# Performance work log

Measured on AMD Instinct MI355X. Metric: run time of the kernel, lower is better.

Reference implementation:

```python
import jax, jax.numpy as jnp
import numpy as np

N_COMPONENTS = 16
N_FEATURES = 64
N_SAMPLES = 200000


def setup_inputs() -> dict:
    key = jax.random.key(0)
    k_data, k_means, k_cov = jax.random.split(key, 3)
    data = jax.random.normal(k_data, (N_SAMPLES, N_FEATURES), dtype=jnp.float32)
    weights = jnp.ones((N_COMPONENTS,), dtype=jnp.float32) / N_COMPONENTS
    means = jax.random.normal(k_means, (N_COMPONENTS, N_FEATURES), dtype=jnp.float32)
    # SPD covariances: A A^T / d + I (module inits to identity; use realistic SPD here)
    A = jax.random.normal(k_cov, (N_COMPONENTS, N_FEATURES, N_FEATURES), dtype=jnp.float32)
    covariances = jnp.einsum('kij,klj->kil', A, A) / N_FEATURES + jnp.eye(N_FEATURES, dtype=jnp.float32)
    return {"data": data, "weights": weights, "means": means, "covariances": covariances}


def reference(data, weights, means, covariances):
    # data: [N, d]; weights: [K]; means: [K, d]; covariances: [K, d, d]
    d = data.shape[1]
    L = jnp.linalg.cholesky(covariances)                      # [K, d, d]
    diff = data[None, :, :] - means[:, None, :]               # [K, N, d]
    # Solve L y = diff^T per component (batched triangular solve)
    y = jax.scipy.linalg.solve_triangular(L, jnp.swapaxes(diff, -1, -2), lower=True)  # [K, d, N]
    maha = jnp.sum(y * y, axis=1)                             # [K, N]
    half_logdet = jnp.sum(jnp.log(jnp.diagonal(L, axis1=-2, axis2=-1)), axis=-1)      # [K]
    log2pi = jnp.log(jnp.array(2.0 * np.pi, dtype=data.dtype))
    log_probs = -0.5 * (maha + d * log2pi) - half_logdet[:, None]                     # [K, N]
    weighted_log_probs = log_probs + jnp.log(weights)[:, None]
    log_sum_exp = jax.scipy.special.logsumexp(weighted_log_probs, axis=0)             # [N]
    return jnp.sum(log_sum_exp)
```

## Files before the change

### kernel.cpp

```cpp
#include <hip/hip_runtime.h>
#include <hip/hip_bf16.h>
#include <math.h>

#define NF 64
#define NC 16
#define MAIN_BLOCKS 256
#define MAIN_WAVES  13
#define TPW 4

typedef __bf16 bf16x8 __attribute__((ext_vector_type(8)));
typedef float f32x4 __attribute__((ext_vector_type(4)));
typedef unsigned int u32;

__device__ __forceinline__ void stage16(const void* gsrc, void* ldst) {
    __builtin_amdgcn_global_load_lds(
        (const __attribute__((address_space(1))) u32*)gsrc,
        (__attribute__((address_space(3))) u32*)ldst,
        16, 0, 0);
}

__device__ __forceinline__ float xor32_sum(float x) {
    float a = x, b = x;
    asm("v_permlane32_swap_b32 %0, %1" : "+v"(a), "+v"(b));
    return a + b;
}
__device__ __forceinline__ float xor16_sum(float x) {
    float a = x, b = x;
    asm("v_permlane16_swap_b32 %0, %1" : "+v"(a), "+v"(b));
    return a + b;
}

__global__ __launch_bounds__(256) void gmm_precompute(
    const float* __restrict__ cov,
    const float* __restrict__ means,
    const float* __restrict__ weights,
    __hip_bfloat16* __restrict__ g,
    float* __restrict__ t,
    float* __restrict__ Cc)
{
    const int w = threadIdx.x >> 6;
    const int c = threadIdx.x & 63;
    const int k = blockIdx.x;

    __shared__ __align__(16) float LT[NF][68];
    __shared__ float Xs[NF][65];
    __shared__ __align__(16) float wb2[2][68];
    __shared__ __align__(16) float gw2[2][68];

    float a_loc[16];
    {
        const float* src = cov + (long)k * NF * NF + (w * 16) * NF + c;
        #pragma unroll
        for (int r = 0; r < 16; ++r)
            a_loc[r] = src[r * NF];
    }

    float rsq_loc[16];
    float logdiag = 0.0f;

    #pragma unroll 1
    for (int q = 0; q < 4; ++q) {
        #pragma unroll
        for (int jj = 0; jj < 16; ++jj) {
            float* wb = wb2[jj & 1];
            if (w == q) wb[c] = a_loc[jj];
            __syncthreads();
            const int j = q * 16 + jj;
            float ajc = wb[c];
            float d   = wb[j];
            float sq  = sqrtf(d);
            float rsq = __builtin_amdgcn_rcpf(sq);
            float rd  = __builtin_amdgcn_rcpf(d);
            logdiag += 0.5f * __logf(d);
            if (w == q) rsq_loc[jj] = rsq;
            LT[j][c] = ajc * rsq;
            float beta = ajc * rd;
            const float4* wv = (const float4*)(wb + w * 16);
            #pragma unroll
            for (int rr = 0; rr < 16; rr += 4) {
                float4 v = wv[rr >> 2];
                a_loc[rr]     = fmaf(-v.x, beta, a_loc[rr]);
                a_loc[rr + 1] = fmaf(-v.y, beta, a_loc[rr + 1]);
                a_loc[rr + 2] = fmaf(-v.z, beta, a_loc[rr + 2]);
                a_loc[rr + 3] = fmaf(-v.w, beta, a_loc[rr + 3]);
            }
        }
    }

    float s_loc[16];
    #pragma unroll
    for (int r = 0; r < 16; ++r)
        s_loc[r] = (w * 16 + r == c) ? 1.0f : 0.0f;

    #pragma unroll 1
    for (int q = 0; q < 4; ++q) {
        #pragma unroll
        for (int ii = 0; ii < 16; ++ii) {
            const int i = q * 16 + ii;
            float* gw = gw2[ii & 1];
            if (w == q) {
                float gv = s_loc[ii] * rsq_loc[ii];
                gw[c] = gv;
                Xs[i][c] = gv;
            }
            __syncthreads();
            float gc = gw[c];
            const float4* lv4 = (const float4*)(&LT[i][w * 16]);
            #pragma unroll
            for (int rr = 0; rr < 16; rr += 4) {
                float4 v = lv4[rr >> 2];
                s_loc[rr]     = fmaf(-v.x, gc, s_loc[rr]);
                s_loc[rr + 1] = fmaf(-v.y, gc, s_loc[rr + 1]);
                s_loc[rr + 2] = fmaf(-v.z, gc, s_loc[rr + 2]);
                s_loc[rr + 3] = fmaf(-v.w, gc, s_loc[rr + 3]);
            }
        }
    }
    __syncthreads();

    {
        __hip_bfloat16* grow = g + ((long)(k * NF + c)) * NF;
        #pragma unroll
        for (int h = 0; h < 2; ++h) {
            int jb = w * 2 + h;
            bf16x8 v;
            #pragma unroll
            for (int u = 0; u < 8; ++u)
                v[u] = (__bf16)Xs[c][jb * 8 + u];
            *(bf16x8*)(grow + ((jb ^ (c & 7)) * 8)) = v;
        }
    }

    if (w == 0) {
        const float* mu = means + k * NF;
        float a0 = 0.0f, a1 = 0.0f;
        #pragma unroll
        for (int j = 0; j < NF; j += 2) {
            a0 = fmaf(Xs[c][j],     mu[j],     a0);
            a1 = fmaf(Xs[c][j + 1], mu[j + 1], a1);
        }
        t[k * NF + c] = a0 + a1;
        if (c == 0)
            Cc[k] = __logf(weights[k]) - 0.5f * (float)NF * 1.8378770664093453f - logdiag;
    }
}

__global__ __launch_bounds__(832) void gmm_main(
    const float* __restrict__ data,
    const char* __restrict__ gsw,
    const float* __restrict__ t,
    const float* __restrict__ Cc,
    float* __restrict__ partials,
    int nTiles, int N, int totalWaves)
{
    __shared__ __align__(16) char gbuf[NC * 8192];
    __shared__ __align__(16) float nt_lds[NC * NF];
    __shared__ float cc_lds[NC];

    const int tidx = threadIdx.x;
    const int w    = tidx >> 6;
    const int lane = tidx & 63;
    const int l15  = lane & 15;
    const int lg   = lane >> 4;

    for (int i = w; i < NC; i += MAIN_WAVES) {
        const char* src = gsw + (size_t)i * 8192;
        char* dst = gbuf + (size_t)i * 8192;
        #pragma unroll
        for (int u = 0; u < 8; ++u)
            stage16(src + u * 1024 + lane * 16, dst + u * 1024);
    }

    for (int i = tidx; i < NC * NF; i += 64 * MAIN_WAVES) nt_lds[i] = -t[i];
    if (tidx < NC) cc_lds[tidx] = Cc[tidx];

    const int gid = blockIdx.x * MAIN_WAVES + w;

    int offA[4], offB[4];
    #pragma unroll
    for (int rc = 0; rc < 4; ++rc) {
        int row = rc * 16 + l15;
        offA[rc] = row * 128 + ((lg       ^ (l15 & 7)) * 16);
        offB[rc] = row * 128 + (((lg + 4) ^ (l15 & 7)) * 16);
    }

    bf16x8 xf[TPW][2];
    if (gid < nTiles) {
        const long base = (long)gid * (TPW * 16);
        #pragma unroll
        for (int st = 0; st < TPW; ++st) {
            long row = base + st * 16 + l15;
            if (row > (long)N - 1) row = (long)N - 1;
            const float* xp = data + row * NF + lg * 8;
            float4 a0 = *(const float4*)(xp);
            float4 a1 = *(const float4*)(xp + 4);
            float4 b0 = *(const float4*)(xp + 32);
            float4 b1 = *(const float4*)(xp + 36);
            bf16x8 f0, f1;
            f0[0] = (__bf16)a0.x; f0[1] = (__bf16)a0.y;
            f0[2] = (__bf16)a0.z; f0[3] = (__bf16)a0.w;
            f0[4] = (__bf16)a1.x; f0[5] = (__bf16)a1.y;
            f0[6] = (__bf16)a1.z; f0[7] = (__bf16)a1.w;
            f1[0] = (__bf16)b0.x; f1[1] = (__bf16)b0.y;
            f1[2] = (__bf16)b0.z; f1[3] = (__bf16)b0.w;
            f1[4] = (__bf16)b1.x; f1[5] = (__bf16)b1.y;
            f1[6] = (__bf16)b1.z; f1[7] = (__bf16)b1.w;
            xf[st][0] = f0;
            xf[st][1] = f1;
        }
    }

    __syncthreads();

    float wavePartial = 0.0f;

    #pragma unroll 1
    for (int tile = gid; tile < nTiles; tile += totalWaves) {
        const long base = (long)tile * (TPW * 16);
        if (tile != gid) {
            #pragma unroll
            for (int st = 0; st < TPW; ++st) {
                long row = base + st * 16 + l15;
                if (row > (long)N - 1) row = (long)N - 1;
                const float* xp = data + row * NF + lg * 8;
                float4 a0 = *(const float4*)(xp);
                float4 a1 = *(const float4*)(xp + 4);
                float4 b0 = *(const float4*)(xp + 32);
                float4 b1 = *(const float4*)(xp + 36);
                bf16x8 f0, f1;
                f0[0] = (__bf16)a0.x; f0[1] = (__bf16)a0.y;
                f0[2] = (__bf16)a0.z; f0[3] = (__bf16)a0.w;
                f0[4] = (__bf16)a1.x; f0[5] = (__bf16)a1.y;
                f0[6] = (__bf16)a1.z; f0[7] = (__bf16)a1.w;
                f1[0] = (__bf16)b0.x; f1[1] = (__bf16)b0.y;
                f1[2] = (__bf16)b0.z; f1[3] = (__bf16)b0.w;
                f1[4] = (__bf16)b1.x; f1[5] = (__bf16)b1.y;
                f1[6] = (__bf16)b1.z; f1[7] = (__bf16)b1.w;
                xf[st][0] = f0;
                xf[st][1] = f1;
            }
        }

        float m[TPW], s[TPW];
        #pragma unroll
        for (int st = 0; st < TPW; ++st) { m[st] = -INFINITY; s[st] = 0.0f; }

        #pragma unroll 2
        for (int ii = 0; ii < NC; ++ii) {
            const int kk = (ii + w) & (NC - 1);
            float mah[TPW];
            #pragma unroll
            for (int st = 0; st < TPW; ++st) mah[st] = 0.0f;

            const char* gk = gbuf + kk * 8192;
            const float* ntk = &nt_lds[kk * NF];

            #pragma unroll
            for (int rc = 0; rc < 2; ++rc) {
                bf16x8 ga = *(const bf16x8*)(gk + offA[rc]);
                f32x4 ntv = *(const f32x4*)(ntk + rc * 16 + lg * 4);
                #pragma unroll
                for (int st = 0; st < TPW; ++st) {
                    f32x4 acc = ntv;
                    acc = __builtin_amdgcn_mfma_f32_16x16x32_bf16(ga, xf[st][0], acc, 0, 0, 0);
                    mah[st] = fmaf(acc[0], acc[0], mah[st]);
                    mah[st] = fmaf(acc[1], acc[1], mah[st]);
                    mah[st] = fmaf(acc[2], acc[2], mah[st]);
                    mah[st] = fmaf(acc[3], acc[3], mah[st]);
                }
            }
            #pragma unroll
            for (int rc = 2; rc < 4; ++rc) {
                bf16x8 ga = *(const bf16x8*)(gk + offA[rc]);
                bf16x8 gb = *(const bf16x8*)(gk + offB[rc]);
                f32x4 ntv = *(const f32x4*)(ntk + rc * 16 + lg * 4);
                #pragma unroll
                for (int st = 0; st < TPW; ++st) {
                    f32x4 acc = ntv;
                    acc = __builtin_amdgcn_mfma_f32_16x16x32_bf16(ga, xf[st][0], acc, 0, 0, 0);
                    acc = __builtin_amdgcn_mfma_f32_16x16x32_bf16(gb, xf[st][1], acc, 0, 0, 0);
                    mah[st] = fmaf(acc[0], acc[0], mah[st]);
                    mah[st] = fmaf(acc[1], acc[1], mah[st]);
                    mah[st] = fmaf(acc[2], acc[2], mah[st]);
                    mah[st] = fmaf(acc[3], acc[3], mah[st]);
                }
            }

            float Ck = cc_lds[kk];
            #pragma unroll
            for (int st = 0; st < TPW; ++st) {
                float v = xor32_sum(xor16_sum(mah[st]));
                float wlp = fmaf(-0.5f, v, Ck);
                float mo = m[st];
                float mn = fmaxf(mo, wlp);
                s[st] = s[st] * __expf(mo - mn) + __expf(wlp - mn);
                m[st] = mn;
            }
        }

        if (lg == 0) {
            #pragma unroll
            for (int st = 0; st < TPW; ++st) {
                long sid = base + st * 16 + l15;
                if (sid < (long)N)
                    wavePartial += m[st] + __logf(s[st]);
            }
        }
    }

    #pragma unroll
    for (int off = 1; off < 64; off <<= 1)
        wavePartial += __shfl_xor(wavePartial, off);
    if (lane == 0)
        partials[gid] = wavePartial;
}

__global__ __launch_bounds__(256) void gmm_reduce(
    const float* __restrict__ partials, int n, float* __restrict__ out)
{
    float s = 0.0f;
    for (int i = threadIdx.x; i < n; i += 256)
        s += partials[i];
    #pragma unroll
    for (int off = 1; off < 64; off <<= 1)
        s += __shfl_xor(s, off);
    __shared__ float sm[4];
    const int wave = threadIdx.x >> 6;
    const int lane = threadIdx.x & 63;
    if (lane == 0) sm[wave] = s;
    __syncthreads();
    if (threadIdx.x == 0)
        out[0] = (sm[0] + sm[1]) + (sm[2] + sm[3]);
}

extern "C" void kernel_launch(void* const* d_in, const int* in_sizes, int n_in,
                              void* d_out, int out_size, void* d_ws, size_t ws_size,
                              hipStream_t stream)
{
    const float* data    = (const float*)d_in[0];
    const float* weights = (const float*)d_in[1];
    const float* means   = (const float*)d_in[2];
    const float* cov     = (const float*)d_in[3];

    const int N = in_sizes[0] / NF;

    char* ws = (char*)d_ws;
    __hip_bfloat16* g = (__hip_bfloat16*)ws;
    float* t          = (float*)(ws + 131072);
    float* Cc         = (float*)(ws + 131072 + 4096);
    float* partials   = (float*)(ws + 131072 + 4096 + 64);

    const int nTiles     = (N + TPW * 16 - 1) / (TPW * 16);
    const int totalWaves = MAIN_BLOCKS * MAIN_WAVES;

    gmm_precompute<<<NC, 256, 0, stream>>>(cov, means, weights, g, t, Cc);
    gmm_main<<<MAIN_BLOCKS, 64 * MAIN_WAVES, 0, stream>>>(
        data, (const char*)g, t, Cc, partials, nTiles, N, totalWaves);
    gmm_reduce<<<1, 256, 0, stream>>>(partials, totalWaves, (float*)d_out);
}
```

Baseline: 67.92 us.

## Split mixture components across paired blocks and merge per-sample logsumexp

Each main block now handles only half of the mixture components (8 instead of 16). Blocks are paired, so twice as many blocks run, each staging half the whitening matrices into LDS. Each half writes a per-sample partial logsumexp to workspace, and a new kernel combines the two halves and reduces. This halves LDS use per block so more blocks can be resident, but it reads the data twice and adds a kernel launch plus per-sample global writes and reads.

```diff
diff --git a/kernel.cpp b/kernel.cpp
--- a/kernel.cpp
+++ b/kernel.cpp
@@ -4,7 +4,8 @@
 
 #define NF 64
 #define NC 16
-#define MAIN_BLOCKS 256
+#define HC 8
+#define MAIN_GROUPS 256
 #define MAIN_WAVES  13
 #define TPW 4
 
@@ -145,36 +146,38 @@
     }
 }
 
-__global__ __launch_bounds__(832) void gmm_main(
+__global__ __launch_bounds__(832, 7) void gmm_main(
     const float* __restrict__ data,
     const char* __restrict__ gsw,
     const float* __restrict__ t,
     const float* __restrict__ Cc,
-    float* __restrict__ partials,
+    float* __restrict__ lseP,
     int nTiles, int N, int totalWaves)
 {
-    __shared__ __align__(16) char gbuf[NC * 8192];
-    __shared__ __align__(16) float nt_lds[NC * NF];
-    __shared__ float cc_lds[NC];
+    __shared__ __align__(16) char gbuf[HC * 8192];
+    __shared__ __align__(16) float nt_lds[HC * NF];
+    __shared__ float cc_lds[HC];
 
     const int tidx = threadIdx.x;
     const int w    = tidx >> 6;
     const int lane = tidx & 63;
     const int l15  = lane & 15;
     const int lg   = lane >> 4;
-
-    for (int i = w; i < NC; i += MAIN_WAVES) {
-        const char* src = gsw + (size_t)i * 8192;
-        char* dst = gbuf + (size_t)i * 8192;
+    const int half = blockIdx.x & 1;
+    const int grp  = blockIdx.x >> 1;
+
+    if (w < HC) {
+        const char* src = gsw + (size_t)(half * HC + w) * 8192;
+        char* dst = gbuf + (size_t)w * 8192;
         #pragma unroll
         for (int u = 0; u < 8; ++u)
             stage16(src + u * 1024 + lane * 16, dst + u * 1024);
     }
-
-    for (int i = tidx; i < NC * NF; i += 64 * MAIN_WAVES) nt_lds[i] = -t[i];
-    if (tidx < NC) cc_lds[tidx] = Cc[tidx];
-
-    const int gid = blockIdx.x * MAIN_WAVES + w;
+    for (int i = tidx; i < HC * NF; i += 64 * MAIN_WAVES)
+        nt_lds[i] = -t[half * HC * NF + i];
+    if (tidx < HC) cc_lds[tidx] = Cc[half * HC + tidx];
+
+    const int gid = grp * MAIN_WAVES + w;
 
     int offA[4], offB[4];
     #pragma unroll
@@ -212,8 +215,6 @@
 
     __syncthreads();
 
-    float wavePartial = 0.0f;
-
     #pragma unroll 1
     for (int tile = gid; tile < nTiles; tile += totalWaves) {
         const long base = (long)tile * (TPW * 16);
@@ -246,8 +247,8 @@
         for (int st = 0; st < TPW; ++st) { m[st] = -INFINITY; s[st] = 0.0f; }
 
         #pragma unroll 2
-        for (int ii = 0; ii < NC; ++ii) {
-            const int kk = (ii + w) & (NC - 1);
+        for (int ii = 0; ii < HC; ++ii) {
+            const int kk = (ii + w) & (HC - 1);
             float mah[TPW];
             #pragma unroll
             for (int st = 0; st < TPW; ++st) mah[st] = 0.0f;
@@ -299,20 +300,36 @@
         }
 
         if (lg == 0) {
+            float* dst = lseP + (size_t)half * 64 * nTiles + (size_t)tile * 64;
             #pragma unroll
             for (int st = 0; st < TPW; ++st) {
                 long sid = base + st * 16 + l15;
                 if (sid < (long)N)
-                    wavePartial += m[st] + __logf(s[st]);
-            }
-        }
-    }
-
+                    dst[st * 16 + l15] = m[st] + __logf(s[st]);
+            }
+        }
+    }
+}
+
+__global__ __launch_bounds__(256) void gmm_partial(
+    const float* __restrict__ lseP, int nTiles, int N,
+    float* __restrict__ blockPartials)
+{
+    const float* h1 = lseP + (size_t)64 * nTiles;
+    float acc = 0.0f;
+    for (int sid = blockIdx.x * 256 + threadIdx.x; sid < N; sid += 256 * 256) {
+        float a = lseP[sid], b = h1[sid];
+        float M = fmaxf(a, b);
+        acc += M + __logf(__expf(a - M) + __expf(b - M));
+    }
     #pragma unroll
     for (int off = 1; off < 64; off <<= 1)
-        wavePartial += __shfl_xor(wavePartial, off);
-    if (lane == 0)
-        partials[gid] = wavePartial;
+        acc += __shfl_xor(acc, off);
+    __shared__ float sm[4];
+    if ((threadIdx.x & 63) == 0) sm[threadIdx.x >> 6] = acc;
+    __syncthreads();
+    if (threadIdx.x == 0)
+        blockPartials[blockIdx.x] = (sm[0] + sm[1]) + (sm[2] + sm[3]);
 }
 
 __global__ __launch_bounds__(256) void gmm_reduce(
@@ -344,17 +361,19 @@
 
     const int N = in_sizes[0] / NF;
 
+    const int nTiles     = (N + TPW * 16 - 1) / (TPW * 16);
+    const int totalWaves = MAIN_GROUPS * MAIN_WAVES;
+
     char* ws = (char*)d_ws;
     __hip_bfloat16* g = (__hip_bfloat16*)ws;
     float* t          = (float*)(ws + 131072);
     float* Cc         = (float*)(ws + 131072 + 4096);
-    float* partials   = (float*)(ws + 131072 + 4096 + 64);
-
-    const int nTiles     = (N + TPW * 16 - 1) / (TPW * 16);
-    const int totalWaves = MAIN_BLOCKS * MAIN_WAVES;
+    float* lseP       = (float*)(ws + 131072 + 4096 + 64);
+    float* blockPartials = lseP + (size_t)2 * nTiles * 64;
 
     gmm_precompute<<<NC, 256, 0, stream>>>(cov, means, weights, g, t, Cc);
-    gmm_main<<<MAIN_BLOCKS, 64 * MAIN_WAVES, 0, stream>>>(
-        data, (const char*)g, t, Cc, partials, nTiles, N, totalWaves);
-    gmm_reduce<<<1, 256, 0, stream>>>(partials, totalWaves, (float*)d_out);
-}
+    gmm_main<<<MAIN_GROUPS * 2, 64 * MAIN_WAVES, 0, stream>>>(
+        data, (const char*)g, t, Cc, lseP, nTiles, N, totalWaves);
+    gmm_partial<<<256, 256, 0, stream>>>(lseP, nTiles, N, blockPartials);
+    gmm_reduce<<<1, 256, 0, stream>>>(blockPartials, 256, (float*)d_out);
+}
```

After: 88.60 us. 30.5% more time.
